# Kernel optimization log

Hardware: AMD Instinct MI355X
Metric: run time of the kernel (lower is better)

## Reference

```python
import jax, jax.numpy as jnp
import numpy as np

N = 100000   # nodes
E = 1600000  # edges
G = 512      # graphs in batch
EPS = 1e-5


def gcn_conv(x, W, b, src, dst, n):
    # PyG GCNConv: h = x W; add self-loops; norm = deg^-1/2[src] * deg^-1/2[dst]
    h = x @ W                                                    # [N, H]
    deg = jax.ops.segment_sum(jnp.ones((src.shape[0],), h.dtype), dst,
                              num_segments=n) + 1.0              # +1 for self-loop
    dis = jax.lax.rsqrt(deg)                                     # deg > 0 always (self-loop)
    coef = (dis[src] * dis[dst])[:, None]                        # [E, 1]
    agg = jax.ops.segment_sum(h[src] * coef, dst, num_segments=n)
    agg = agg + h * (dis * dis)[:, None]                         # self-loop term
    return agg + b


def bn_relu(x, gamma, beta):
    # BatchNorm1d in training mode: batch stats, biased variance
    mu = jnp.mean(x, axis=0)
    var = jnp.mean(jnp.square(x - mu), axis=0)
    xn = (x - mu) * jax.lax.rsqrt(var + EPS)
    return jax.nn.relu(xn * gamma + beta)


def setup_inputs() -> dict:
    key = jax.random.key(0)
    ks = jax.random.split(key, 16)
    F_in, H, C = 128, 64, 10
    x = jax.random.normal(ks[0], (N, F_in), dtype=jnp.float32)
    edge_index = jax.random.randint(ks[1], (2, E), 0, N, dtype=jnp.int64)
    batch = jnp.sort(jax.random.randint(ks[2], (N,), 0, G, dtype=jnp.int64))
    def lin(k, fi, fo):
        s = 1.0 / np.sqrt(fi)
        kw, kb = jax.random.split(k)
        return (jax.random.uniform(kw, (fi, fo), jnp.float32, -s, s),
                jax.random.uniform(kb, (fo,), jnp.float32, -s, s))
    W1, b1 = lin(ks[3], F_in, H)
    W2, b2 = lin(ks[4], H, H)
    W3, b3 = lin(ks[5], H, H)
    W4, b4 = lin(ks[6], H, H)
    fcW, fcb = lin(ks[7], H, C)
    ones = jnp.ones((H,), jnp.float32)
    zeros = jnp.zeros((H,), jnp.float32)
    return dict(x=x, edge_index=edge_index, batch=batch,
                W1=W1, b1=b1, g1=ones, bt1=zeros,
                W2=W2, b2=b2, g2=ones, bt2=zeros,
                W3=W3, b3=b3, g3=ones, bt3=zeros,
                W4=W4, b4=b4, g4=ones, bt4=zeros,
                fcW=fcW, fcb=fcb)


def reference(x, edge_index, batch,
              W1, b1, g1, bt1, W2, b2, g2, bt2,
              W3, b3, g3, bt3, W4, b4, g4, bt4, fcW, fcb):
    src, dst = edge_index[0], edge_index[1]
    n = x.shape[0]
    h = bn_relu(gcn_conv(x, W1, b1, src, dst, n), g1, bt1)
    h = bn_relu(gcn_conv(h, W2, b2, src, dst, n), g2, bt2)
    h = bn_relu(gcn_conv(h, W3, b3, src, dst, n), g3, bt3)
    h = bn_relu(gcn_conv(h, W4, b4, src, dst, n), g4, bt4)
    # global mean pool over graphs
    sums = jax.ops.segment_sum(h, batch, num_segments=G)            # [G, H]
    cnts = jax.ops.segment_sum(jnp.ones((n,), h.dtype), batch, num_segments=G)
    pooled = sums / jnp.maximum(cnts, 1.0)[:, None]
    logits = pooled @ fcW + fcb
    return jax.nn.log_softmax(logits, axis=-1)
```

## Files before the change

kernel.cpp:

```cpp
#include <hip/hip_runtime.h>
#include <hip/hip_bf16.h>

#define EPSV 1e-5f
#define BSH 6

struct alignas(8) bf4 { __hip_bfloat16 x,y,z,w; };

__global__ __launch_bounds__(256) void k_bhist(const int* __restrict__ dst, int E, int nb,
                                               int* __restrict__ bhist){
  extern __shared__ int lh[];
  for (int t = threadIdx.x; t < nb; t += 256) lh[t] = 0;
  __syncthreads();
  for (int e = blockIdx.x*256+threadIdx.x; e < E; e += gridDim.x*256)
    atomicAdd(&lh[dst[e]>>BSH], 1);
  __syncthreads();
  for (int t = threadIdx.x; t < nb; t += 256){ int v = lh[t]; if (v) atomicAdd(&bhist[t], v); }
}

__global__ __launch_bounds__(256) void k_bscan(const int* __restrict__ bhist, int nb,
                                               int* __restrict__ boff, int* __restrict__ bcur,
                                               int* __restrict__ rowptr, int n, int E){
  __shared__ int sh[2][256];
  int tid = threadIdx.x;
  int per = (nb + 255) / 256;
  int base = tid*per;
  int v[8]; int s = 0;
  for (int j=0;j<per;++j){ int i=base+j; v[j] = (i<nb)? bhist[i]:0; s += v[j]; }
  sh[0][tid] = s; __syncthreads();
  int pa = 0;
  for (int off=1; off<256; off<<=1){
    int add = (tid>=off)? sh[pa][tid-off] : 0;
    sh[pa^1][tid] = sh[pa][tid] + add;
    pa ^= 1; __syncthreads();
  }
  int run = sh[pa][tid] - s;
  for (int j=0;j<per;++j){ int i=base+j; if (i<nb){ boff[i]=run; bcur[i]=run; run += v[j]; } }
  if (tid==255) boff[nb] = E;
  if (tid==254) rowptr[n] = E;
}

__global__ __launch_bounds__(256) void k_bscatter(const int* __restrict__ src, const int* __restrict__ dst,
                                                  int E, int nb, int nchunk,
                                                  int* __restrict__ bcur, unsigned* __restrict__ ebuf){
  extern __shared__ int lh[];
  int s = blockIdx.x*nchunk, e = min(E, s+nchunk);
  for (int t = threadIdx.x; t < nb; t += 256) lh[t] = 0;
  __syncthreads();
  for (int i = s+threadIdx.x; i < e; i += 256) atomicAdd(&lh[dst[i]>>BSH], 1);
  __syncthreads();
  for (int t = threadIdx.x; t < nb; t += 256){
    int v = lh[t];
    lh[t] = v ? atomicAdd(&bcur[t], v) : 0;
  }
  __syncthreads();
  for (int i = s+threadIdx.x; i < e; i += 256){
    int d = dst[i];
    int pos = atomicAdd(&lh[d>>BSH], 1);
    ebuf[pos] = (unsigned)src[i] | ((unsigned)(d & 63) << 25);
  }
}

__global__ __launch_bounds__(256) void k_bsort(const unsigned* __restrict__ ebuf, const int* __restrict__ boff,
                                               int n, int* __restrict__ rowptr, int* __restrict__ col,
                                               float* __restrict__ dis){
  __shared__ int cnt[64]; __shared__ int cur[64];
  int b = blockIdx.x;
  int s = boff[b], e = boff[b+1];
  if (threadIdx.x < 64) cnt[threadIdx.x] = 0;
  __syncthreads();
  for (int i = s+threadIdx.x; i < e; i += 256) atomicAdd(&cnt[ebuf[i]>>25], 1);
  __syncthreads();
  if (threadIdx.x < 64){
    int v = cnt[threadIdx.x];
    int inc = v;
    for (int off=1; off<64; off<<=1){ int u = __shfl_up(inc, off); if (threadIdx.x >= off) inc += u; }
    int ex = inc - v;
    cur[threadIdx.x] = s + ex;
    int node = b*64 + threadIdx.x;
    if (node < n){ rowptr[node] = s + ex; dis[node] = rsqrtf((float)(v+1)); }
  }
  __syncthreads();
  for (int i = s+threadIdx.x; i < e; i += 256){
    unsigned w = ebuf[i];
    int pos = atomicAdd(&cur[w>>25], 1);
    col[pos] = (int)(w & 0x1FFFFFFu);
  }
}

__global__ __launch_bounds__(256) void k_gsinit(int* __restrict__ gs, int G, int n){
  for (int t = blockIdx.x*256+threadIdx.x; t<=G; t+=gridDim.x*256) gs[t] = n;
}
__global__ __launch_bounds__(256) void k_gsbound(const int* __restrict__ batch, int n, int* __restrict__ gs){
  for (int i = blockIdx.x*256+threadIdx.x; i<n; i+=gridDim.x*256){
    int b = batch[i];
    int prev = (i==0)? -1 : batch[i-1];
    for (int g = prev+1; g<=b; ++g) gs[g] = i;
  }
}

template<int K, bool BN>
__global__ __launch_bounds__(256) void k_gemm(const float* __restrict__ X, const float* __restrict__ W,
    const float* __restrict__ dis, const float* __restrict__ stats,
    const float* __restrict__ g, const float* __restrict__ bt,
    __hip_bfloat16* __restrict__ out, int n, int ntiles)
{
  __shared__ float4 Wl[K*16];
  __shared__ float2 acS[64];
  for (int t = threadIdx.x; t < K*16; t += 256)
    Wl[t] = reinterpret_cast<const float4*>(W)[t];
  if (BN && threadIdx.x < 64){
    int j = threadIdx.x;
    float fn = (float)n;
    float mu = stats[j]/fn;
    float var = stats[64+j]/fn - mu*mu;
    float a = rsqrtf(var + EPSV) * g[j];
    acS[j] = make_float2(a, bt[j] - mu*a);
  }
  __syncthreads();
  int wave = threadIdx.x>>6, lane = threadIdx.x&63;
  int cg = lane&15, rg = lane>>4;

  for (int tile = blockIdx.x*4+wave; tile < ntiles; tile += gridDim.x*4){
    int r0 = tile*16 + rg*4;
    const float* X0 = X + (size_t)min(r0+0, n-1)*K;
    const float* X1 = X + (size_t)min(r0+1, n-1)*K;
    const float* X2 = X + (size_t)min(r0+2, n-1)*K;
    const float* X3 = X + (size_t)min(r0+3, n-1)*K;
    float4 a0 = make_float4(0.f,0.f,0.f,0.f);
    float4 a1 = a0, a2 = a0, a3 = a0;
    float4 c0 = *reinterpret_cast<const float4*>(X0);
    float4 c1 = *reinterpret_cast<const float4*>(X1);
    float4 c2 = *reinterpret_cast<const float4*>(X2);
    float4 c3 = *reinterpret_cast<const float4*>(X3);
    #pragma unroll 2
    for (int k=0; k<K-4; k+=4){
      float4 n0 = *reinterpret_cast<const float4*>(X0 + k + 4);
      float4 n1 = *reinterpret_cast<const float4*>(X1 + k + 4);
      float4 n2 = *reinterpret_cast<const float4*>(X2 + k + 4);
      float4 n3 = *reinterpret_cast<const float4*>(X3 + k + 4);
      float4 w0 = Wl[(k+0)*16+cg];
      float4 w1 = Wl[(k+1)*16+cg];
      float4 w2 = Wl[(k+2)*16+cg];
      float4 w3 = Wl[(k+3)*16+cg];
      if (BN){
        float2 p0 = acS[k], p1 = acS[k+1], p2 = acS[k+2], p3 = acS[k+3];
        c0.x = fmaxf(fmaf(c0.x,p0.x,p0.y),0.f); c0.y = fmaxf(fmaf(c0.y,p1.x,p1.y),0.f);
        c0.z = fmaxf(fmaf(c0.z,p2.x,p2.y),0.f); c0.w = fmaxf(fmaf(c0.w,p3.x,p3.y),0.f);
        c1.x = fmaxf(fmaf(c1.x,p0.x,p0.y),0.f); c1.y = fmaxf(fmaf(c1.y,p1.x,p1.y),0.f);
        c1.z = fmaxf(fmaf(c1.z,p2.x,p2.y),0.f); c1.w = fmaxf(fmaf(c1.w,p3.x,p3.y),0.f);
        c2.x = fmaxf(fmaf(c2.x,p0.x,p0.y),0.f); c2.y = fmaxf(fmaf(c2.y,p1.x,p1.y),0.f);
        c2.z = fmaxf(fmaf(c2.z,p2.x,p2.y),0.f); c2.w = fmaxf(fmaf(c2.w,p3.x,p3.y),0.f);
        c3.x = fmaxf(fmaf(c3.x,p0.x,p0.y),0.f); c3.y = fmaxf(fmaf(c3.y,p1.x,p1.y),0.f);
        c3.z = fmaxf(fmaf(c3.z,p2.x,p2.y),0.f); c3.w = fmaxf(fmaf(c3.w,p3.x,p3.y),0.f);
      }
      a0.x = fmaf(c0.w,w3.x, fmaf(c0.z,w2.x, fmaf(c0.y,w1.x, fmaf(c0.x,w0.x, a0.x))));
      a0.y = fmaf(c0.w,w3.y, fmaf(c0.z,w2.y, fmaf(c0.y,w1.y, fmaf(c0.x,w0.y, a0.y))));
      a0.z = fmaf(c0.w,w3.z, fmaf(c0.z,w2.z, fmaf(c0.y,w1.z, fmaf(c0.x,w0.z, a0.z))));
      a0.w = fmaf(c0.w,w3.w, fmaf(c0.z,w2.w, fmaf(c0.y,w1.w, fmaf(c0.x,w0.w, a0.w))));
      a1.x = fmaf(c1.w,w3.x, fmaf(c1.z,w2.x, fmaf(c1.y,w1.x, fmaf(c1.x,w0.x, a1.x))));
      a1.y = fmaf(c1.w,w3.y, fmaf(c1.z,w2.y, fmaf(c1.y,w1.y, fmaf(c1.x,w0.y, a1.y))));
      a1.z = fmaf(c1.w,w3.z, fmaf(c1.z,w2.z, fmaf(c1.y,w1.z, fmaf(c1.x,w0.z, a1.z))));
      a1.w = fmaf(c1.w,w3.w, fmaf(c1.z,w2.w, fmaf(c1.y,w1.w, fmaf(c1.x,w0.w, a1.w))));
      a2.x = fmaf(c2.w,w3.x, fmaf(c2.z,w2.x, fmaf(c2.y,w1.x, fmaf(c2.x,w0.x, a2.x))));
      a2.y = fmaf(c2.w,w3.y, fmaf(c2.z,w2.y, fmaf(c2.y,w1.y, fmaf(c2.x,w0.y, a2.y))));
      a2.z = fmaf(c2.w,w3.z, fmaf(c2.z,w2.z, fmaf(c2.y,w1.z, fmaf(c2.x,w0.z, a2.z))));
      a2.w = fmaf(c2.w,w3.w, fmaf(c2.z,w2.w, fmaf(c2.y,w1.w, fmaf(c2.x,w0.w, a2.w))));
      a3.x = fmaf(c3.w,w3.x, fmaf(c3.z,w2.x, fmaf(c3.y,w1.x, fmaf(c3.x,w0.x, a3.x))));
      a3.y = fmaf(c3.w,w3.y, fmaf(c3.z,w2.y, fmaf(c3.y,w1.y, fmaf(c3.x,w0.y, a3.y))));
      a3.z = fmaf(c3.w,w3.z, fmaf(c3.z,w2.z, fmaf(c3.y,w1.z, fmaf(c3.x,w0.z, a3.z))));
      a3.w = fmaf(c3.w,w3.w, fmaf(c3.z,w2.w, fmaf(c3.y,w1.w, fmaf(c3.x,w0.w, a3.w))));
      c0 = n0; c1 = n1; c2 = n2; c3 = n3;
    }
    {
      const int k = K-4;
      float4 w0 = Wl[(k+0)*16+cg];
      float4 w1 = Wl[(k+1)*16+cg];
      float4 w2 = Wl[(k+2)*16+cg];
      float4 w3 = Wl[(k+3)*16+cg];
      if (BN){
        float2 p0 = acS[k], p1 = acS[k+1], p2 = acS[k+2], p3 = acS[k+3];
        c0.x = fmaxf(fmaf(c0.x,p0.x,p0.y),0.f); c0.y = fmaxf(fmaf(c0.y,p1.x,p1.y),0.f);
        c0.z = fmaxf(fmaf(c0.z,p2.x,p2.y),0.f); c0.w = fmaxf(fmaf(c0.w,p3.x,p3.y),0.f);
        c1.x = fmaxf(fmaf(c1.x,p0.x,p0.y),0.f); c1.y = fmaxf(fmaf(c1.y,p1.x,p1.y),0.f);
        c1.z = fmaxf(fmaf(c1.z,p2.x,p2.y),0.f); c1.w = fmaxf(fmaf(c1.w,p3.x,p3.y),0.f);
        c2.x = fmaxf(fmaf(c2.x,p0.x,p0.y),0.f); c2.y = fmaxf(fmaf(c2.y,p1.x,p1.y),0.f);
        c2.z = fmaxf(fmaf(c2.z,p2.x,p2.y),0.f); c2.w = fmaxf(fmaf(c2.w,p3.x,p3.y),0.f);
        c3.x = fmaxf(fmaf(c3.x,p0.x,p0.y),0.f); c3.y = fmaxf(fmaf(c3.y,p1.x,p1.y),0.f);
        c3.z = fmaxf(fmaf(c3.z,p2.x,p2.y),0.f); c3.w = fmaxf(fmaf(c3.w,p3.x,p3.y),0.f);
      }
      a0.x = fmaf(c0.w,w3.x, fmaf(c0.z,w2.x, fmaf(c0.y,w1.x, fmaf(c0.x,w0.x, a0.x))));
      a0.y = fmaf(c0.w,w3.y, fmaf(c0.z,w2.y, fmaf(c0.y,w1.y, fmaf(c0.x,w0.y, a0.y))));
      a0.z = fmaf(c0.w,w3.z, fmaf(c0.z,w2.z, fmaf(c0.y,w1.z, fmaf(c0.x,w0.z, a0.z))));
      a0.w = fmaf(c0.w,w3.w, fmaf(c0.z,w2.w, fmaf(c0.y,w1.w, fmaf(c0.x,w0.w, a0.w))));
      a1.x = fmaf(c1.w,w3.x, fmaf(c1.z,w2.x, fmaf(c1.y,w1.x, fmaf(c1.x,w0.x, a1.x))));
      a1.y = fmaf(c1.w,w3.y, fmaf(c1.z,w2.y, fmaf(c1.y,w1.y, fmaf(c1.x,w0.y, a1.y))));
      a1.z = fmaf(c1.w,w3.z, fmaf(c1.z,w2.z, fmaf(c1.y,w1.z, fmaf(c1.x,w0.z, a1.z))));
      a1.w = fmaf(c1.w,w3.w, fmaf(c1.z,w2.w, fmaf(c1.y,w1.w, fmaf(c1.x,w0.w, a1.w))));
      a2.x = fmaf(c2.w,w3.x, fmaf(c2.z,w2.x, fmaf(c2.y,w1.x, fmaf(c2.x,w0.x, a2.x))));
      a2.y = fmaf(c2.w,w3.y, fmaf(c2.z,w2.y, fmaf(c2.y,w1.y, fmaf(c2.x,w0.y, a2.y))));
      a2.z = fmaf(c2.w,w3.z, fmaf(c2.z,w2.z, fmaf(c2.y,w1.z, fmaf(c2.x,w0.z, a2.z))));
      a2.w = fmaf(c2.w,w3.w, fmaf(c2.z,w2.w, fmaf(c2.y,w1.w, fmaf(c2.x,w0.w, a2.w))));
      a3.x = fmaf(c3.w,w3.x, fmaf(c3.z,w2.x, fmaf(c3.y,w1.x, fmaf(c3.x,w0.x, a3.x))));
      a3.y = fmaf(c3.w,w3.y, fmaf(c3.z,w2.y, fmaf(c3.y,w1.y, fmaf(c3.x,w0.y, a3.y))));
      a3.z = fmaf(c3.w,w3.z, fmaf(c3.z,w2.z, fmaf(c3.y,w1.z, fmaf(c3.x,w0.z, a3.z))));
      a3.w = fmaf(c3.w,w3.w, fmaf(c3.z,w2.w, fmaf(c3.y,w1.w, fmaf(c3.x,w0.w, a3.w))));
    }
    if (r0+0 < n){ float d = dis[r0+0];
      bf4 o{__float2bfloat16(a0.x*d),__float2bfloat16(a0.y*d),__float2bfloat16(a0.z*d),__float2bfloat16(a0.w*d)};
      *reinterpret_cast<bf4*>(out + (size_t)(r0+0)*64 + cg*4) = o; }
    if (r0+1 < n){ float d = dis[r0+1];
      bf4 o{__float2bfloat16(a1.x*d),__float2bfloat16(a1.y*d),__float2bfloat16(a1.z*d),__float2bfloat16(a1.w*d)};
      *reinterpret_cast<bf4*>(out + (size_t)(r0+1)*64 + cg*4) = o; }
    if (r0+2 < n){ float d = dis[r0+2];
      bf4 o{__float2bfloat16(a2.x*d),__float2bfloat16(a2.y*d),__float2bfloat16(a2.z*d),__float2bfloat16(a2.w*d)};
      *reinterpret_cast<bf4*>(out + (size_t)(r0+2)*64 + cg*4) = o; }
    if (r0+3 < n){ float d = dis[r0+3];
      bf4 o{__float2bfloat16(a3.x*d),__float2bfloat16(a3.y*d),__float2bfloat16(a3.z*d),__float2bfloat16(a3.w*d)};
      *reinterpret_cast<bf4*>(out + (size_t)(r0+3)*64 + cg*4) = o; }
  }
}

__global__ __launch_bounds__(256) void k_agg(const __hip_bfloat16* __restrict__ H, const int* __restrict__ rp,
    const int* __restrict__ col, const float* __restrict__ dis, const float* __restrict__ bias,
    float* __restrict__ out, float* __restrict__ stats, int n)
{
  int wave = threadIdx.x>>6, lane = threadIdx.x&63;
  float bj = bias[lane];
  float bsum = 0.f, bsq = 0.f;
  int nw = gridDim.x*4;
  for (int i = blockIdx.x*4+wave; i<n; i+=nw){
    int s = rp[i], e = rp[i+1];
    float acc = __bfloat162float(H[(size_t)i*64+lane]);
    int t = s;
    for (; t+8 <= e; t += 8){
      int c0 = col[t],   c1 = col[t+1], c2 = col[t+2], c3 = col[t+3];
      int c4 = col[t+4], c5 = col[t+5], c6 = col[t+6], c7 = col[t+7];
      float v0 = __bfloat162float(H[(size_t)c0*64+lane]);
      float v1 = __bfloat162float(H[(size_t)c1*64+lane]);
      float v2 = __bfloat162float(H[(size_t)c2*64+lane]);
      float v3 = __bfloat162float(H[(size_t)c3*64+lane]);
      float v4 = __bfloat162float(H[(size_t)c4*64+lane]);
      float v5 = __bfloat162float(H[(size_t)c5*64+lane]);
      float v6 = __bfloat162float(H[(size_t)c6*64+lane]);
      float v7 = __bfloat162float(H[(size_t)c7*64+lane]);
      acc += ((v0+v1)+(v2+v3)) + ((v4+v5)+(v6+v7));
    }
    for (; t+4 <= e; t += 4){
      int c0 = col[t], c1 = col[t+1], c2 = col[t+2], c3 = col[t+3];
      float v0 = __bfloat162float(H[(size_t)c0*64+lane]);
      float v1 = __bfloat162float(H[(size_t)c1*64+lane]);
      float v2 = __bfloat162float(H[(size_t)c2*64+lane]);
      float v3 = __bfloat162float(H[(size_t)c3*64+lane]);
      acc += (v0+v1)+(v2+v3);
    }
    for (; t<e; ++t) acc += __bfloat162float(H[(size_t)col[t]*64+lane]);
    float v = fmaf(dis[i], acc, bj);
    out[(size_t)i*64+lane] = v;
    bsum += v; bsq = fmaf(v, v, bsq);
  }
  __shared__ float red[2][4][64];
  red[0][wave][lane] = bsum; red[1][wave][lane] = bsq;
  __syncthreads();
  if (wave==0){
    float s0 = (red[0][0][lane]+red[0][1][lane]) + (red[0][2][lane]+red[0][3][lane]);
    float q0 = (red[1][0][lane]+red[1][1][lane]) + (red[1][2][lane]+red[1][3][lane]);
    atomicAdd(&stats[lane], s0);
    atomicAdd(&stats[64+lane], q0);
  }
}

__global__ __launch_bounds__(256) void k_pool(const float* __restrict__ agg, const float* __restrict__ stats,
                                              const float* __restrict__ g, const float* __restrict__ bt,
                                              const int* __restrict__ gs, float* __restrict__ pooled, int n){
  __shared__ float2 acS[64];
  if (threadIdx.x < 64){
    int j = threadIdx.x;
    float fn = (float)n;
    float mu = stats[j]/fn;
    float var = stats[64+j]/fn - mu*mu;
    float a = rsqrtf(var + EPSV) * g[j];
    acS[j] = make_float2(a, bt[j] - mu*a);
  }
  __syncthreads();
  int gr = blockIdx.x;
  int s = gs[gr], e = gs[gr+1];
  int wave = threadIdx.x>>6, lane = threadIdx.x&63;
  float a = acS[lane].x, c = acS[lane].y;
  float acc = 0.f;
  for (int i = s+wave; i < e; i += 4)
    acc += fmaxf(fmaf(agg[(size_t)i*64+lane], a, c), 0.f);
  __shared__ float red[4][64];
  red[wave][lane] = acc; __syncthreads();
  if (wave==0){
    float t = (red[0][lane]+red[1][lane]) + (red[2][lane]+red[3][lane]);
    float cg = (float)(e - s);
    pooled[(size_t)gr*64+lane] = t / fmaxf(cg, 1.f);
  }
}

__global__ __launch_bounds__(256) void k_logits(const float* __restrict__ pooled, const float* __restrict__ fcW,
                                                const float* __restrict__ fcb, float* __restrict__ out, int G){
  int gw = (blockIdx.x*256 + threadIdx.x) >> 6;
  int lane = threadIdx.x & 63;
  if (gw >= G) return;
  float l = -1e30f;
  if (lane < 10){
    l = fcb[lane];
    for (int k=0;k<64;++k) l = fmaf(pooled[(size_t)gw*64+k], fcW[k*10+lane], l);
  }
  float m = l;
  for (int off=32; off; off>>=1) m = fmaxf(m, __shfl_xor(m, off));
  float ex = (lane<10)? expf(l-m) : 0.f;
  float ssum = ex;
  for (int off=32; off; off>>=1) ssum += __shfl_xor(ssum, off);
  if (lane < 10) out[(size_t)gw*10+lane] = l - m - logf(ssum);
}

extern "C" void kernel_launch(void* const* d_in, const int* in_sizes, int n_in,
                              void* d_out, int out_size, void* d_ws, size_t ws_size,
                              hipStream_t stream){
  const float* x    = (const float*)d_in[0];
  const int*   ei   = (const int*)d_in[1];
  const int*   batch= (const int*)d_in[2];
  const float* W1 = (const float*)d_in[3];  const float* b1 = (const float*)d_in[4];
  const float* g1 = (const float*)d_in[5];  const float* bt1= (const float*)d_in[6];
  const float* W2 = (const float*)d_in[7];  const float* b2 = (const float*)d_in[8];
  const float* g2 = (const float*)d_in[9];  const float* bt2= (const float*)d_in[10];
  const float* W3 = (const float*)d_in[11]; const float* b3 = (const float*)d_in[12];
  const float* g3 = (const float*)d_in[13]; const float* bt3= (const float*)d_in[14];
  const float* W4 = (const float*)d_in[15]; const float* b4 = (const float*)d_in[16];
  const float* g4 = (const float*)d_in[17]; const float* bt4= (const float*)d_in[18];
  const float* fcW= (const float*)d_in[19]; const float* fcb= (const float*)d_in[20];

  int n = in_sizes[0] / 128;
  int E = in_sizes[1] / 2;
  int G = out_size / 10;
  const int* src = ei;
  const int* dst = ei + E;
  int nb = (n + 63) >> 6;

  char* p = (char*)d_ws;
  auto alloc = [&](size_t bytes)->void*{ void* r = p; p += (bytes + 255) & ~(size_t)255; return r; };
  int*   bhist  = (int*)  alloc((size_t)nb*4);
  int*   boff   = (int*)  alloc((size_t)(nb+1)*4);
  int*   bcur   = (int*)  alloc((size_t)nb*4);
  int*   rowptr = (int*)  alloc((size_t)(n+1)*4);
  int*   col    = (int*)  alloc((size_t)E*4);
  float* dis    = (float*)alloc((size_t)n*4);
  __hip_bfloat16* bufB = (__hip_bfloat16*)alloc((size_t)n*64*2);
  float* bufC   = (float*)alloc((size_t)n*64*4);
  float* stats  = (float*)alloc(4*128*4);
  int*   gs     = (int*)  alloc((size_t)(G+1)*4);
  float* pooled = (float*)alloc((size_t)G*64*4);
  unsigned* ebuf = (unsigned*)bufB;

  hipMemsetAsync(bhist, 0, (size_t)nb*4, stream);
  hipMemsetAsync(stats, 0, 4*128*4, stream);

  size_t ldsb = (size_t)nb*4;
  k_bhist<<<256,256,ldsb,stream>>>(dst, E, nb, bhist);
  k_bscan<<<1,256,0,stream>>>(bhist, nb, boff, bcur, rowptr, n, E);
  int nchunk = (E + 255) / 256;
  k_bscatter<<<256,256,ldsb,stream>>>(src, dst, E, nb, nchunk, bcur, ebuf);
  k_bsort<<<nb,256,0,stream>>>(ebuf, boff, n, rowptr, col, dis);
  k_gsinit<<<4,256,0,stream>>>(gs, G, n);
  k_gsbound<<<512,256,0,stream>>>(batch, n, gs);

  int ntiles = (n + 15) / 16;
  int gg  = (ntiles + 3) / 4;

  k_gemm<128,false><<<gg,256,0,stream>>>(x, W1, dis, nullptr, nullptr, nullptr, bufB, n, ntiles);
  k_agg<<<2048,256,0,stream>>>(bufB, rowptr, col, dis, b1, bufC, stats+0, n);
  k_gemm<64,true><<<gg,256,0,stream>>>(bufC, W2, dis, stats+0, g2, bt2, bufB, n, ntiles);
  k_agg<<<2048,256,0,stream>>>(bufB, rowptr, col, dis, b2, bufC, stats+128, n);
  k_gemm<64,true><<<gg,256,0,stream>>>(bufC, W3, dis, stats+128, g3, bt3, bufB, n, ntiles);
  k_agg<<<2048,256,0,stream>>>(bufB, rowptr, col, dis, b3, bufC, stats+256, n);
  k_gemm<64,true><<<gg,256,0,stream>>>(bufC, W4, dis, stats+256, g4, bt4, bufB, n, ntiles);
  k_agg<<<2048,256,0,stream>>>(bufB, rowptr, col, dis, b4, bufC, stats+384, n);

  k_pool<<<G,256,0,stream>>>(bufC, stats+384, g4, bt4, gs, pooled, n);
  k_logits<<<(G*64 + 255)/256,256,0,stream>>>(pooled, fcW, fcb, (float*)d_out, G);
}
```

Before: 568.1 us.

## Split bf16 features into four 16-column planes and aggregate per plane

The GEMM now writes its bf16 output as four column-quarter planes of 16 features each ([4][n][16]), not row-major [n][64]. The new aggregation kernel assigns each block to one plane, so each plane (about 3.2 MB) is more likely to stay in cache during the random neighbor gathers. Within a wave, four slots of 16 lanes each gather a different neighbor, and the partial sums are combined with shuffles. The costs are 32-byte gather granularity, redundant rowptr/col reads across the four planes, and a quarter of lanes idle in the epilogue.

```diff
diff --git a/kernel.cpp b/kernel.cpp
--- a/kernel.cpp
+++ b/kernel.cpp
@@ -119,6 +119,8 @@
   __syncthreads();
   int wave = threadIdx.x>>6, lane = threadIdx.x&63;
   int cg = lane&15, rg = lane>>4;
+  int qq = cg>>2;
+  size_t qbase = (size_t)qq*n*16 + (cg&3)*4;
 
   for (int tile = blockIdx.x*4+wave; tile < ntiles; tile += gridDim.x*4){
     int r0 = tile*16 + rg*4;
@@ -207,65 +209,64 @@
     }
     if (r0+0 < n){ float d = dis[r0+0];
       bf4 o{__float2bfloat16(a0.x*d),__float2bfloat16(a0.y*d),__float2bfloat16(a0.z*d),__float2bfloat16(a0.w*d)};
-      *reinterpret_cast<bf4*>(out + (size_t)(r0+0)*64 + cg*4) = o; }
+      *reinterpret_cast<bf4*>(out + qbase + (size_t)(r0+0)*16) = o; }
     if (r0+1 < n){ float d = dis[r0+1];
       bf4 o{__float2bfloat16(a1.x*d),__float2bfloat16(a1.y*d),__float2bfloat16(a1.z*d),__float2bfloat16(a1.w*d)};
-      *reinterpret_cast<bf4*>(out + (size_t)(r0+1)*64 + cg*4) = o; }
+      *reinterpret_cast<bf4*>(out + qbase + (size_t)(r0+1)*16) = o; }
     if (r0+2 < n){ float d = dis[r0+2];
       bf4 o{__float2bfloat16(a2.x*d),__float2bfloat16(a2.y*d),__float2bfloat16(a2.z*d),__float2bfloat16(a2.w*d)};
-      *reinterpret_cast<bf4*>(out + (size_t)(r0+2)*64 + cg*4) = o; }
+      *reinterpret_cast<bf4*>(out + qbase + (size_t)(r0+2)*16) = o; }
     if (r0+3 < n){ float d = dis[r0+3];
       bf4 o{__float2bfloat16(a3.x*d),__float2bfloat16(a3.y*d),__float2bfloat16(a3.z*d),__float2bfloat16(a3.w*d)};
-      *reinterpret_cast<bf4*>(out + (size_t)(r0+3)*64 + cg*4) = o; }
-  }
-}
-
-__global__ __launch_bounds__(256) void k_agg(const __hip_bfloat16* __restrict__ H, const int* __restrict__ rp,
+      *reinterpret_cast<bf4*>(out + qbase + (size_t)(r0+3)*16) = o; }
+  }
+}
+
+__global__ __launch_bounds__(256) void k_agg4(const __hip_bfloat16* __restrict__ H, const int* __restrict__ rp,
     const int* __restrict__ col, const float* __restrict__ dis, const float* __restrict__ bias,
     float* __restrict__ out, float* __restrict__ stats, int n)
 {
   int wave = threadIdx.x>>6, lane = threadIdx.x&63;
-  float bj = bias[lane];
-  float bsum = 0.f, bsq = 0.f;
-  int nw = gridDim.x*4;
-  for (int i = blockIdx.x*4+wave; i<n; i+=nw){
+  int slot = lane>>4, ch = lane&15;
+  int q  = (blockIdx.x & 7) >> 1;
+  int ib = ((blockIdx.x >> 3) << 1) | (blockIdx.x & 1);
+  const __hip_bfloat16* Hq = H + (size_t)q*n*16;
+  float bj = bias[q*16+ch];
+  float bsum=0.f, bsq=0.f;
+  int nw = (gridDim.x>>2)*4;
+  for (int i = ib*4+wave; i<n; i+=nw){
     int s = rp[i], e = rp[i+1];
-    float acc = __bfloat162float(H[(size_t)i*64+lane]);
+    float acc = (slot==0) ? __bfloat162float(Hq[(size_t)i*16+ch]) : 0.f;
     int t = s;
-    for (; t+8 <= e; t += 8){
-      int c0 = col[t],   c1 = col[t+1], c2 = col[t+2], c3 = col[t+3];
-      int c4 = col[t+4], c5 = col[t+5], c6 = col[t+6], c7 = col[t+7];
-      float v0 = __bfloat162float(H[(size_t)c0*64+lane]);
-      float v1 = __bfloat162float(H[(size_t)c1*64+lane]);
-      float v2 = __bfloat162float(H[(size_t)c2*64+lane]);
-      float v3 = __bfloat162float(H[(size_t)c3*64+lane]);
-      float v4 = __bfloat162float(H[(size_t)c4*64+lane]);
-      float v5 = __bfloat162float(H[(size_t)c5*64+lane]);
-      float v6 = __bfloat162float(H[(size_t)c6*64+lane]);
-      float v7 = __bfloat162float(H[(size_t)c7*64+lane]);
-      acc += ((v0+v1)+(v2+v3)) + ((v4+v5)+(v6+v7));
-    }
-    for (; t+4 <= e; t += 4){
-      int c0 = col[t], c1 = col[t+1], c2 = col[t+2], c3 = col[t+3];
-      float v0 = __bfloat162float(H[(size_t)c0*64+lane]);
-      float v1 = __bfloat162float(H[(size_t)c1*64+lane]);
-      float v2 = __bfloat162float(H[(size_t)c2*64+lane]);
-      float v3 = __bfloat162float(H[(size_t)c3*64+lane]);
-      acc += (v0+v1)+(v2+v3);
-    }
-    for (; t<e; ++t) acc += __bfloat162float(H[(size_t)col[t]*64+lane]);
-    float v = fmaf(dis[i], acc, bj);
-    out[(size_t)i*64+lane] = v;
-    bsum += v; bsq = fmaf(v, v, bsq);
-  }
-  __shared__ float red[2][4][64];
-  red[0][wave][lane] = bsum; red[1][wave][lane] = bsq;
-  __syncthreads();
-  if (wave==0){
-    float s0 = (red[0][0][lane]+red[0][1][lane]) + (red[0][2][lane]+red[0][3][lane]);
-    float q0 = (red[1][0][lane]+red[1][1][lane]) + (red[1][2][lane]+red[1][3][lane]);
-    atomicAdd(&stats[lane], s0);
-    atomicAdd(&stats[64+lane], q0);
+    for (; t+8<=e; t+=8){
+      int c0 = col[t+slot];
+      int c1 = col[t+4+slot];
+      float v0 = __bfloat162float(Hq[(size_t)c0*16+ch]);
+      float v1 = __bfloat162float(Hq[(size_t)c1*16+ch]);
+      acc += v0 + v1;
+    }
+    if (t+slot < e){
+      float v = __bfloat162float(Hq[(size_t)col[t+slot]*16+ch]);
+      int t1 = t+4+slot;
+      if (t1 < e) v += __bfloat162float(Hq[(size_t)col[t1]*16+ch]);
+      acc += v;
+    }
+    acc += __shfl_xor(acc,16);
+    acc += __shfl_xor(acc,32);
+    if (slot==0){
+      float v = fmaf(dis[i], acc, bj);
+      out[(size_t)i*64 + q*16 + ch] = v;
+      bsum += v; bsq = fmaf(v,v,bsq);
+    }
+  }
+  __shared__ float red[2][4][16];
+  if (slot==0){ red[0][wave][ch]=bsum; red[1][wave][ch]=bsq; }
+  __syncthreads();
+  if (wave==0 && lane<16){
+    float s0 = (red[0][0][lane]+red[0][1][lane])+(red[0][2][lane]+red[0][3][lane]);
+    float q0 = (red[1][0][lane]+red[1][1][lane])+(red[1][2][lane]+red[1][3][lane]);
+    atomicAdd(&stats[q*16+lane], s0);
+    atomicAdd(&stats[64+q*16+lane], q0);
   }
 }
 
@@ -370,13 +371,13 @@
   int gg  = (ntiles + 3) / 4;
 
   k_gemm<128,false><<<gg,256,0,stream>>>(x, W1, dis, nullptr, nullptr, nullptr, bufB, n, ntiles);
-  k_agg<<<2048,256,0,stream>>>(bufB, rowptr, col, dis, b1, bufC, stats+0, n);
+  k_agg4<<<2048,256,0,stream>>>(bufB, rowptr, col, dis, b1, bufC, stats+0, n);
   k_gemm<64,true><<<gg,256,0,stream>>>(bufC, W2, dis, stats+0, g2, bt2, bufB, n, ntiles);
-  k_agg<<<2048,256,0,stream>>>(bufB, rowptr, col, dis, b2, bufC, stats+128, n);
+  k_agg4<<<2048,256,0,stream>>>(bufB, rowptr, col, dis, b2, bufC, stats+128, n);
   k_gemm<64,true><<<gg,256,0,stream>>>(bufC, W3, dis, stats+128, g3, bt3, bufB, n, ntiles);
-  k_agg<<<2048,256,0,stream>>>(bufB, rowptr, col, dis, b3, bufC, stats+256, n);
+  k_agg4<<<2048,256,0,stream>>>(bufB, rowptr, col, dis, b3, bufC, stats+256, n);
   k_gemm<64,true><<<gg,256,0,stream>>>(bufC, W4, dis, stats+256, g4, bt4, bufB, n, ntiles);
-  k_agg<<<2048,256,0,stream>>>(bufB, rowptr, col, dis, b4, bufC, stats+384, n);
+  k_agg4<<<2048,256,0,stream>>>(bufB, rowptr, col, dis, b4, bufC, stats+384, n);
 
   k_pool<<<G,256,0,stream>>>(bufC, stats+384, g4, bt4, gs, pooled, n);
   k_logits<<<(G*64 + 255)/256,256,0,stream>>>(pooled, fcW, fcb, (float*)d_out, G);
```

Measured after the change: 682.7 us. 1.2x slower.

## Partition neighbor lists by source quarter and aggregate in source-range phases

Applied to the files above, without the earlier changes.

The CSR build now splits each node's neighbor list into four buckets by source-node range and records the split offsets per node. The aggregation kernel processes a fixed set of up to 13 nodes per wave in four phases, each gathering only sources from one quarter of the node range, with partial sums kept in shared memory. The aim is to shrink the working set of gathered feature rows per phase so they stay in cache. The cost is extra shared memory, a split-offset array, and less dynamic load balance because each wave owns a fixed node set.

```diff
diff --git a/kernel.cpp b/kernel.cpp
--- a/kernel.cpp
+++ b/kernel.cpp
@@ -3,6 +3,7 @@
 
 #define EPSV 1e-5f
 #define BSH 6
+#define NPW 13
 
 struct alignas(8) bf4 { __hip_bfloat16 x,y,z,w; };
 
@@ -62,28 +63,45 @@
 
 __global__ __launch_bounds__(256) void k_bsort(const unsigned* __restrict__ ebuf, const int* __restrict__ boff,
                                                int n, int* __restrict__ rowptr, int* __restrict__ col,
-                                               float* __restrict__ dis){
-  __shared__ int cnt[64]; __shared__ int cur[64];
+                                               float* __restrict__ dis, ushort4* __restrict__ splits){
+  __shared__ int cnt[64][4]; __shared__ int cur[64][4];
   int b = blockIdx.x;
   int s = boff[b], e = boff[b+1];
-  if (threadIdx.x < 64) cnt[threadIdx.x] = 0;
-  __syncthreads();
-  for (int i = s+threadIdx.x; i < e; i += 256) atomicAdd(&cnt[ebuf[i]>>25], 1);
-  __syncthreads();
-  if (threadIdx.x < 64){
-    int v = cnt[threadIdx.x];
-    int inc = v;
-    for (int off=1; off<64; off<<=1){ int u = __shfl_up(inc, off); if (threadIdx.x >= off) inc += u; }
-    int ex = inc - v;
-    cur[threadIdx.x] = s + ex;
-    int node = b*64 + threadIdx.x;
-    if (node < n){ rowptr[node] = s + ex; dis[node] = rsqrtf((float)(v+1)); }
-  }
+  int q1 = n>>2, q2 = n>>1, q3 = (n>>2) + (n>>1);
+  if (threadIdx.x < 64){ cnt[threadIdx.x][0]=0; cnt[threadIdx.x][1]=0; cnt[threadIdx.x][2]=0; cnt[threadIdx.x][3]=0; }
   __syncthreads();
   for (int i = s+threadIdx.x; i < e; i += 256){
     unsigned w = ebuf[i];
-    int pos = atomicAdd(&cur[w>>25], 1);
-    col[pos] = (int)(w & 0x1FFFFFFu);
+    int node = w>>25;
+    int sc = (int)(w & 0x1FFFFFFu);
+    int q = (sc>=q1) + (sc>=q2) + (sc>=q3);
+    atomicAdd(&cnt[node][q], 1);
+  }
+  __syncthreads();
+  if (threadIdx.x < 64){
+    int node = threadIdx.x;
+    int v0=cnt[node][0], v1=cnt[node][1], v2=cnt[node][2], v3=cnt[node][3];
+    int v = v0+v1+v2+v3;
+    int inc = v;
+    for (int off=1; off<64; off<<=1){ int u = __shfl_up(inc, off); if (node >= off) inc += u; }
+    int ex = inc - v;
+    int base = s + ex;
+    cur[node][0]=base; cur[node][1]=base+v0; cur[node][2]=base+v0+v1; cur[node][3]=base+v0+v1+v2;
+    int gnode = b*64 + node;
+    if (gnode < n){
+      rowptr[gnode] = base;
+      dis[gnode] = rsqrtf((float)(v+1));
+      splits[gnode] = make_ushort4((ushort)v0, (ushort)(v0+v1), (ushort)(v0+v1+v2), 0);
+    }
+  }
+  __syncthreads();
+  for (int i = s+threadIdx.x; i < e; i += 256){
+    unsigned w = ebuf[i];
+    int node = w>>25;
+    int sc = (int)(w & 0x1FFFFFFu);
+    int q = (sc>=q1) + (sc>=q2) + (sc>=q3);
+    int pos = atomicAdd(&cur[node][q], 1);
+    col[pos] = sc;
   }
 }
 
@@ -221,42 +239,65 @@
 }
 
 __global__ __launch_bounds__(256) void k_agg(const __hip_bfloat16* __restrict__ H, const int* __restrict__ rp,
-    const int* __restrict__ col, const float* __restrict__ dis, const float* __restrict__ bias,
+    const int* __restrict__ col, const ushort4* __restrict__ splits,
+    const float* __restrict__ dis, const float* __restrict__ bias,
     float* __restrict__ out, float* __restrict__ stats, int n)
 {
+  __shared__ float accS[4][NPW][64];
   int wave = threadIdx.x>>6, lane = threadIdx.x&63;
+  int wid = blockIdx.x*4 + wave;
+  int nw = gridDim.x*4;
+  #pragma unroll
+  for (int j=0;j<NPW;++j){
+    int i = wid + j*nw;
+    accS[wave][j][lane] = (i<n) ? __bfloat162float(H[(size_t)i*64+lane]) : 0.f;
+  }
+  for (int p=0;p<4;++p){
+    for (int j=0;j<NPW;++j){
+      int i = wid + j*nw;
+      if (i>=n) break;
+      int base = rp[i];
+      ushort4 sp = splits[i];
+      int o0 = (p==0)? 0 : (p==1? sp.x : (p==2? sp.y : sp.z));
+      int o1 = (p==3)? (rp[i+1]-base) : (p==0? sp.x : (p==1? sp.y : sp.z));
+      int s = base + o0, e = base + o1;
+      float acc = 0.f;
+      int t = s;
+      for (; t+8 <= e; t += 8){
+        int c0 = col[t],   c1 = col[t+1], c2 = col[t+2], c3 = col[t+3];
+        int c4 = col[t+4], c5 = col[t+5], c6 = col[t+6], c7 = col[t+7];
+        float v0 = __bfloat162float(H[(size_t)c0*64+lane]);
+        float v1 = __bfloat162float(H[(size_t)c1*64+lane]);
+        float v2 = __bfloat162float(H[(size_t)c2*64+lane]);
+        float v3 = __bfloat162float(H[(size_t)c3*64+lane]);
+        float v4 = __bfloat162float(H[(size_t)c4*64+lane]);
+        float v5 = __bfloat162float(H[(size_t)c5*64+lane]);
+        float v6 = __bfloat162float(H[(size_t)c6*64+lane]);
+        float v7 = __bfloat162float(H[(size_t)c7*64+lane]);
+        acc += ((v0+v1)+(v2+v3)) + ((v4+v5)+(v6+v7));
+      }
+      for (; t+4 <= e; t += 4){
+        int c0 = col[t], c1 = col[t+1], c2 = col[t+2], c3 = col[t+3];
+        float v0 = __bfloat162float(H[(size_t)c0*64+lane]);
+        float v1 = __bfloat162float(H[(size_t)c1*64+lane]);
+        float v2 = __bfloat162float(H[(size_t)c2*64+lane]);
+        float v3 = __bfloat162float(H[(size_t)c3*64+lane]);
+        acc += (v0+v1)+(v2+v3);
+      }
+      for (; t<e; ++t) acc += __bfloat162float(H[(size_t)col[t]*64+lane]);
+      accS[wave][j][lane] += acc;
+    }
+  }
   float bj = bias[lane];
   float bsum = 0.f, bsq = 0.f;
-  int nw = gridDim.x*4;
-  for (int i = blockIdx.x*4+wave; i<n; i+=nw){
-    int s = rp[i], e = rp[i+1];
-    float acc = __bfloat162float(H[(size_t)i*64+lane]);
-    int t = s;
-    for (; t+8 <= e; t += 8){
-      int c0 = col[t],   c1 = col[t+1], c2 = col[t+2], c3 = col[t+3];
-      int c4 = col[t+4], c5 = col[t+5], c6 = col[t+6], c7 = col[t+7];
-      float v0 = __bfloat162float(H[(size_t)c0*64+lane]);
-      float v1 = __bfloat162float(H[(size_t)c1*64+lane]);
-      float v2 = __bfloat162float(H[(size_t)c2*64+lane]);
-      float v3 = __bfloat162float(H[(size_t)c3*64+lane]);
-      float v4 = __bfloat162float(H[(size_t)c4*64+lane]);
-      float v5 = __bfloat162float(H[(size_t)c5*64+lane]);
-      float v6 = __bfloat162float(H[(size_t)c6*64+lane]);
-      float v7 = __bfloat162float(H[(size_t)c7*64+lane]);
-      acc += ((v0+v1)+(v2+v3)) + ((v4+v5)+(v6+v7));
+  #pragma unroll
+  for (int j=0;j<NPW;++j){
+    int i = wid + j*nw;
+    if (i<n){
+      float v = fmaf(dis[i], accS[wave][j][lane], bj);
+      out[(size_t)i*64+lane] = v;
+      bsum += v; bsq = fmaf(v, v, bsq);
     }
-    for (; t+4 <= e; t += 4){
-      int c0 = col[t], c1 = col[t+1], c2 = col[t+2], c3 = col[t+3];
-      float v0 = __bfloat162float(H[(size_t)c0*64+lane]);
-      float v1 = __bfloat162float(H[(size_t)c1*64+lane]);
-      float v2 = __bfloat162float(H[(size_t)c2*64+lane]);
-      float v3 = __bfloat162float(H[(size_t)c3*64+lane]);
-      acc += (v0+v1)+(v2+v3);
-    }
-    for (; t<e; ++t) acc += __bfloat162float(H[(size_t)col[t]*64+lane]);
-    float v = fmaf(dis[i], acc, bj);
-    out[(size_t)i*64+lane] = v;
-    bsum += v; bsq = fmaf(v, v, bsq);
   }
   __shared__ float red[2][4][64];
   red[0][wave][lane] = bsum; red[1][wave][lane] = bsq;
@@ -346,6 +387,7 @@
   int*   bcur   = (int*)  alloc((size_t)nb*4);
   int*   rowptr = (int*)  alloc((size_t)(n+1)*4);
   int*   col    = (int*)  alloc((size_t)E*4);
+  ushort4* splits = (ushort4*)alloc((size_t)n*8);
   float* dis    = (float*)alloc((size_t)n*4);
   __hip_bfloat16* bufB = (__hip_bfloat16*)alloc((size_t)n*64*2);
   float* bufC   = (float*)alloc((size_t)n*64*4);
@@ -362,21 +404,23 @@
   k_bscan<<<1,256,0,stream>>>(bhist, nb, boff, bcur, rowptr, n, E);
   int nchunk = (E + 255) / 256;
   k_bscatter<<<256,256,ldsb,stream>>>(src, dst, E, nb, nchunk, bcur, ebuf);
-  k_bsort<<<nb,256,0,stream>>>(ebuf, boff, n, rowptr, col, dis);
+  k_bsort<<<nb,256,0,stream>>>(ebuf, boff, n, rowptr, col, dis, splits);
   k_gsinit<<<4,256,0,stream>>>(gs, G, n);
   k_gsbound<<<512,256,0,stream>>>(batch, n, gs);
 
   int ntiles = (n + 15) / 16;
   int gg  = (ntiles + 3) / 4;
+  int ab = (n + 4*NPW - 1) / (4*NPW);
+  if (ab < 2048) ab = 2048;
 
   k_gemm<128,false><<<gg,256,0,stream>>>(x, W1, dis, nullptr, nullptr, nullptr, bufB, n, ntiles);
-  k_agg<<<2048,256,0,stream>>>(bufB, rowptr, col, dis, b1, bufC, stats+0, n);
+  k_agg<<<ab,256,0,stream>>>(bufB, rowptr, col, splits, dis, b1, bufC, stats+0, n);
   k_gemm<64,true><<<gg,256,0,stream>>>(bufC, W2, dis, stats+0, g2, bt2, bufB, n, ntiles);
-  k_agg<<<2048,256,0,stream>>>(bufB, rowptr, col, dis, b2, bufC, stats+128, n);
+  k_agg<<<ab,256,0,stream>>>(bufB, rowptr, col, splits, dis, b2, bufC, stats+128, n);
   k_gemm<64,true><<<gg,256,0,stream>>>(bufC, W3, dis, stats+128, g3, bt3, bufB, n, ntiles);
-  k_agg<<<2048,256,0,stream>>>(bufB, rowptr, col, dis, b3, bufC, stats+256, n);
+  k_agg<<<ab,256,0,stream>>>(bufB, rowptr, col, splits, dis, b3, bufC, stats+256, n);
   k_gemm<64,true><<<gg,256,0,stream>>>(bufC, W4, dis, stats+256, g4, bt4, bufB, n, ntiles);
-  k_agg<<<2048,256,0,stream>>>(bufB, rowptr, col, dis, b4, bufC, stats+384, n);
+  k_agg<<<ab,256,0,stream>>>(bufB, rowptr, col, splits, dis, b4, bufC, stats+384, n);
 
   k_pool<<<G,256,0,stream>>>(bufC, stats+384, g4, bt4, gs, pooled, n);
   k_logits<<<(G*64 + 255)/256,256,0,stream>>>(pooled, fcW, fcb, (float*)d_out, G);
```

Measured after the change: 761.6 us. 34.1% more time.
